# Optimization experiments

Measured on AMD Instinct MI355X. Metric: run time of the kernel, lower is better.

## Reference

```python
import jax, jax.numpy as jnp
import numpy as np

N, E, H, B = 100000, 1600000, 64, 256
EPS = 1e-5


def ln(x, g, b):
    mu = jnp.mean(x, axis=-1, keepdims=True)
    var = jnp.mean((x - mu) ** 2, axis=-1, keepdims=True)
    return (x - mu) * jax.lax.rsqrt(var + EPS) * g + b


def gelu(x):
    # torch nn.GELU default is exact (erf) gelu
    return jax.nn.gelu(x, approximate=False)


def setup_inputs() -> dict:
    key = jax.random.key(0)
    ks = iter(jax.random.split(key, 64))
    nk = lambda: next(ks)
    s = 0.1
    p = {}
    p["x"] = jax.random.normal(nk(), (N, 2), jnp.float32)
    p["edge_attr"] = jax.random.normal(nk(), (E, 2), jnp.float32)
    # node_embed: Linear(2,H) LN GELU Linear(H,H) LN GELU (dropout = eval no-op)
    p["ne_w1"] = jax.random.normal(nk(), (2, H), jnp.float32) * s
    p["ne_b1"] = jnp.zeros((H,), jnp.float32)
    p["ne_g1"] = jnp.ones((H,), jnp.float32)
    p["ne_be1"] = jnp.zeros((H,), jnp.float32)
    p["ne_w2"] = jax.random.normal(nk(), (H, H), jnp.float32) * s
    p["ne_b2"] = jnp.zeros((H,), jnp.float32)
    p["ne_g2"] = jnp.ones((H,), jnp.float32)
    p["ne_be2"] = jnp.zeros((H,), jnp.float32)
    # 3 TrackConv layers: message MLP Linear(H+2,H)+LN, conv output LN, and outer per-layer LN
    p["conv_w"] = jax.random.normal(nk(), (3, H + 2, H), jnp.float32) * s
    p["conv_b"] = jnp.zeros((3, H), jnp.float32)
    p["conv_mg"] = jnp.ones((3, H), jnp.float32)
    p["conv_mb"] = jnp.zeros((3, H), jnp.float32)
    p["conv_ng"] = jnp.ones((3, H), jnp.float32)
    p["conv_nb"] = jnp.zeros((3, H), jnp.float32)
    p["out_ng"] = jnp.ones((3, H), jnp.float32)
    p["out_nb"] = jnp.zeros((3, H), jnp.float32)
    # head MLP: Linear(H,H)+LN+ReLU, Linear(H,H//2)+LN+ReLU, Linear(H//2,1)
    p["m_w1"] = jax.random.normal(nk(), (H, H), jnp.float32) * s
    p["m_b1"] = jnp.zeros((H,), jnp.float32)
    p["m_g1"] = jnp.ones((H,), jnp.float32)
    p["m_be1"] = jnp.zeros((H,), jnp.float32)
    p["m_w2"] = jax.random.normal(nk(), (H, H // 2), jnp.float32) * s
    p["m_b2"] = jnp.zeros((H // 2,), jnp.float32)
    p["m_g2"] = jnp.ones((H // 2,), jnp.float32)
    p["m_be2"] = jnp.zeros((H // 2,), jnp.float32)
    p["m_w3"] = jax.random.normal(nk(), (H // 2, 1), jnp.float32) * s
    p["m_b3"] = jnp.zeros((1,), jnp.float32)
    p["edge_index"] = jax.random.randint(nk(), (2, E), 0, N, dtype=jnp.int32)
    p["batch"] = jnp.sort(jax.random.randint(nk(), (N,), 0, B, dtype=jnp.int32))
    return p


def reference(x, edge_attr,
              ne_w1, ne_b1, ne_g1, ne_be1, ne_w2, ne_b2, ne_g2, ne_be2,
              conv_w, conv_b, conv_mg, conv_mb, conv_ng, conv_nb, out_ng, out_nb,
              m_w1, m_b1, m_g1, m_be1, m_w2, m_b2, m_g2, m_be2, m_w3, m_b3,
              edge_index, batch):
    # node embedding (dropout in eval = identity)
    h = gelu(ln(x @ ne_w1 + ne_b1, ne_g1, ne_be1))
    h = gelu(ln(h @ ne_w2 + ne_b2, ne_g2, ne_be2))
    src, dst = edge_index[0], edge_index[1]  # PyG: message from src (x_j), aggregate at dst
    deg = jax.ops.segment_sum(jnp.ones((E,), h.dtype), dst, num_segments=N)
    deg = jnp.maximum(deg, 1.0)[:, None]
    for l in range(3):
        msg_in = jnp.concatenate([h[src], edge_attr], axis=-1)  # [E, H+2]
        msg = gelu(ln(msg_in @ conv_w[l] + conv_b[l], conv_mg[l], conv_mb[l]))  # [E, H]
        agg = jax.ops.segment_sum(msg, dst, num_segments=N) / deg  # mean aggregate
        conv_out = ln(agg + h, conv_ng[l], conv_nb[l])  # TrackConv: norm(out + residual)
        h = h + ln(conv_out, out_ng[l], out_nb[l])  # outer norm + residual
    # global mean pool over graphs
    cnt = jnp.maximum(jax.ops.segment_sum(jnp.ones((N,), h.dtype), batch, num_segments=B), 1.0)[:, None]
    g = jax.ops.segment_sum(h, batch, num_segments=B) / cnt  # [B, H]
    g = jax.nn.relu(ln(g @ m_w1 + m_b1, m_g1, m_be1))
    g = jax.nn.relu(ln(g @ m_w2 + m_b2, m_g2, m_be2))
    return g @ m_w3 + m_b3  # [B, 1]
```

## Files before the change

### kernel.cpp

```cpp
#include <hip/hip_runtime.h>
#include <math.h>


typedef __attribute__((ext_vector_type(8))) short bfrag;
typedef __attribute__((ext_vector_type(4))) float ffrag;

template <int CTRL>
__device__ __forceinline__ float dpp_mov(float v) {
  return __int_as_float(
      __builtin_amdgcn_update_dpp(0, __float_as_int(v), CTRL, 0xF, 0xF, true));
}

__device__ __forceinline__ float rsum16(float v) {
  v += dpp_mov<0x128>(v);
  v += dpp_mov<0x124>(v);
  v += dpp_mov<0x122>(v);
  v += dpp_mov<0x121>(v);
  return v;
}

__device__ __forceinline__ float wave_sum64(float v) {
  v = rsum16(v);
  v += __shfl_xor(v, 16, 64);
  v += __shfl_xor(v, 32, 64);
  return v;
}

__device__ __forceinline__ float ln_apply(float t, float g, float b) {
  float mu = wave_sum64(t) * 0.015625f;
  float d = t - mu;
  float var = wave_sum64(d * d) * 0.015625f;
  return d * rsqrtf(var + 1e-5f) * g + b;
}

__device__ __forceinline__ float erf_fast(float x) {
  float ax = fabsf(x);
  float p = fmaf(fmaf(fmaf(fmaf(0.078108f, ax, 0.000972f), ax, 0.230389f),
                      ax, 0.278393f), ax, 1.0f);
  p = p * p;
  p = p * p;
  float r = __builtin_amdgcn_rcpf(p);
  return copysignf(1.0f - r, x);
}

__device__ __forceinline__ float gelu_exact(float v) {
  float half = 0.5f * v;
  return fmaf(half, erf_fast(v * 0.70710678118654752440f), half);
}

__device__ __forceinline__ float lane_bcast(float v, int k) {
  return __uint_as_float(__builtin_amdgcn_readlane(__float_as_uint(v), k));
}

__device__ __forceinline__ short f2bf(float f) {
  union { float f; unsigned u; } v; v.f = f;
  unsigned r = v.u + 0x7fffu + ((v.u >> 16) & 1u);
  return (short)(r >> 16);
}

__global__ __launch_bounds__(256) void k_init(
    const float* __restrict__ x,
    const float* __restrict__ w1, const float* __restrict__ b1,
    const float* __restrict__ g1, const float* __restrict__ be1,
    const float* __restrict__ w2, const float* __restrict__ b2,
    const float* __restrict__ g2, const float* __restrict__ be2,
    const float* __restrict__ conv_w, ushort* __restrict__ wt,
    const int* __restrict__ ei, int* __restrict__ csr,
    float* __restrict__ h, ushort* __restrict__ hb,
    int n_nodes, int ne, int oHist, int oEmb, int embWaves) {
  const int bid = blockIdx.x;
  const int tid = threadIdx.x;
  if (bid < oHist) {
    const int i = bid * 256 + tid;
    const int k = i % 96, f = (i / 96) % 64, l = i / (96 * 64);
    const float v = (k < 66) ? conv_w[(size_t)l * 66 * 64 + k * 64 + f] : 0.0f;
    wt[i] = (ushort)f2bf(v);
    return;
  }
  if (bid < oEmb) {
    const int i = (bid - oHist) * 256 + tid;
    if (i < ne) atomicAdd(&csr[ei[ne + i]], 1);
    return;
  }
  const int lane = tid & 63;
  const int wid = ((bid - oEmb) * 256 + tid) >> 6;
  const int nw = embWaves;
  float wc[64];
#pragma unroll
  for (int k = 0; k < 64; k++) wc[k] = w2[k * 64 + lane];
  const float w1a = w1[lane], w1b = w1[64 + lane];
  const float vb1 = b1[lane], vg1 = g1[lane], vbe1 = be1[lane];
  const float vb2 = b2[lane], vg2 = g2[lane], vbe2 = be2[lane];
  for (int n = wid; n < n_nodes; n += nw) {
    const float x0 = x[2 * n], x1 = x[2 * n + 1];
    float t = fmaf(x0, w1a, fmaf(x1, w1b, vb1));
    t = gelu_exact(ln_apply(t, vg1, vbe1));
    float a0 = vb2, a1 = 0.f, a2 = 0.f, a3 = 0.f;
#pragma unroll
    for (int k = 0; k < 64; k += 4) {
      a0 = fmaf(lane_bcast(t, k + 0), wc[k + 0], a0);
      a1 = fmaf(lane_bcast(t, k + 1), wc[k + 1], a1);
      a2 = fmaf(lane_bcast(t, k + 2), wc[k + 2], a2);
      a3 = fmaf(lane_bcast(t, k + 3), wc[k + 3], a3);
    }
    float acc = (a0 + a1) + (a2 + a3);
    acc = gelu_exact(ln_apply(acc, vg2, vbe2));
    h[n * 64 + lane] = acc;
    hb[n * 64 + lane] = (ushort)f2bf(acc);
  }
}

__global__ __launch_bounds__(1024) void k_scan_fast(int* __restrict__ buf, int n) {
  __shared__ int wsum[16];
  const int tid = threadIdx.x, lane = tid & 63, w = tid >> 6;
  const int chunk = (((n + 1023) / 1024) + 3) & ~3;
  const int a = min(tid * chunk, n), b = min(a + chunk, n);
  const bool full = (a + chunk <= n);
  int s = 0;
  if (full) {
    const int4* p4 = (const int4*)(buf + a);
#pragma unroll 4
    for (int i = 0; i < chunk / 4; i++) {
      int4 v = p4[i];
      s += v.x + v.y + v.z + v.w;
    }
  } else {
    for (int i = a; i < b; i++) s += buf[i];
  }
  int inc = s;
#pragma unroll
  for (int sh = 1; sh < 64; sh <<= 1) {
    int t = __shfl_up(inc, sh, 64);
    if (lane >= sh) inc += t;
  }
  if (lane == 63) wsum[w] = inc;
  __syncthreads();
  int wb = 0;
  for (int j = 0; j < w; j++) wb += wsum[j];
  int excl = wb + inc - s;
  if (full) {
    int4* p4 = (int4*)(buf + a);
#pragma unroll 4
    for (int i = 0; i < chunk / 4; i++) {
      int4 v = p4[i];
      int4 o;
      o.x = excl; excl += v.x;
      o.y = excl; excl += v.y;
      o.z = excl; excl += v.z;
      o.w = excl; excl += v.w;
      p4[i] = o;
    }
  } else {
    for (int i = a; i < b; i++) { int v = buf[i]; buf[i] = excl; excl += v; }
  }
}

__global__ void k_scatter(const int* __restrict__ ei, const float* __restrict__ ea,
                          int* __restrict__ cursor, int2* __restrict__ edata, int ne) {
  int i = blockIdx.x * blockDim.x + threadIdx.x;
  if (i < ne) {
    const int d = ei[ne + i];
    const int s = ei[i];
    const float2 eav = *(const float2*)(ea + 2 * (size_t)i);
    const unsigned pk = (unsigned)(ushort)f2bf(eav.x) |
                        ((unsigned)(ushort)f2bf(eav.y) << 16);
    const int pos = atomicAdd(&cursor[d], 1);
    edata[pos] = make_int2(s, (int)pk);
  }
}

__global__ __launch_bounds__(1024) void k_edge_node(
    const float* __restrict__ h_in, const ushort* __restrict__ hb_in,
    float* __restrict__ h_out, ushort* __restrict__ hb_out,
    const int2* __restrict__ edata, const int* __restrict__ ends,
    const ushort* __restrict__ wt,
    const float* __restrict__ bias, const float* __restrict__ mg,
    const float* __restrict__ mb,
    const float* __restrict__ ng, const float* __restrict__ nb,
    const float* __restrict__ og, const float* __restrict__ ob,
    int n_nodes, int writeHb) {
  __shared__ __align__(16) ushort lwt[64 * 96];
  {
    const uint4* s = (const uint4*)wt;
    uint4* d = (uint4*)lwt;
    if (threadIdx.x < 768) d[threadIdx.x] = s[threadIdx.x];
  }
  __syncthreads();

  const int lane = threadIdx.x & 63;
  const int grp = lane >> 4, col = lane & 15;
  const int wid = (blockIdx.x * blockDim.x + threadIdx.x) >> 6;
  const int nw = (gridDim.x * blockDim.x) >> 6;

  float vb[4], vg[4], vbb[4];
#pragma unroll
  for (int t = 0; t < 4; t++) {
    const int f = t * 16 + col;
    vb[t] = bias[f]; vg[t] = mg[f]; vbb[t] = mb[f];
  }

  for (int n = wid; n < n_nodes; n += nw) {
    const int start = (n == 0) ? 0 : ends[n - 1];
    const int end = ends[n];
    float aggf[4] = {0.f, 0.f, 0.f, 0.f};

    int p = start;
    int2 ed = edata[p + min(col, end - p - 1)];
    const ushort* hp0 = hb_in + (size_t)ed.x * 64 + grp * 8;
    bfrag A0 = *(const bfrag*)(hp0);
    bfrag A1 = *(const bfrag*)(hp0 + 32);
    int edy = ed.y;

    for (;;) {
      const int rem = min(16, end - p);
      const int pn = p + 16;
      const bool more = pn < end;
      const int nidx = more ? (pn + min(col, end - pn - 1)) : (p + min(col, rem - 1));
      const int2 edn = edata[nidx];

      bfrag A2 = {0, 0, 0, 0, 0, 0, 0, 0};
      if (grp == 0) {
        A2[0] = (short)(edy & 0xffff);
        A2[1] = (short)((unsigned)edy >> 16);
      }

      ffrag acc[4];
#pragma unroll
      for (int t = 0; t < 4; t++) { ffrag c = {vb[t], vb[t], vb[t], vb[t]}; acc[t] = c; }
#pragma unroll
      for (int t = 0; t < 4; t++) {
        const bfrag B = *(const bfrag*)(lwt + (t * 16 + col) * 96 + grp * 8);
        acc[t] = __builtin_amdgcn_mfma_f32_16x16x32_bf16(A0, B, acc[t], 0, 0, 0);
      }
#pragma unroll
      for (int t = 0; t < 4; t++) {
        const bfrag B = *(const bfrag*)(lwt + (t * 16 + col) * 96 + 32 + grp * 8);
        acc[t] = __builtin_amdgcn_mfma_f32_16x16x32_bf16(A1, B, acc[t], 0, 0, 0);
      }
#pragma unroll
      for (int t = 0; t < 4; t++) {
        const bfrag B = *(const bfrag*)(lwt + (t * 16 + col) * 96 + 64 + grp * 8);
        acc[t] = __builtin_amdgcn_mfma_f32_16x16x32_bf16(A2, B, acc[t], 0, 0, 0);
      }

      const ushort* hq = hb_in + (size_t)edn.x * 64 + grp * 8;
      const bfrag N0 = *(const bfrag*)(hq);
      const bfrag N1 = *(const bfrag*)(hq + 32);

      float sx[4], sq[4];
#pragma unroll
      for (int r = 0; r < 4; r++) {
        float s = (acc[0][r] + acc[1][r]) + (acc[2][r] + acc[3][r]);
        float q = fmaf(acc[0][r], acc[0][r], fmaf(acc[1][r], acc[1][r],
                  fmaf(acc[2][r], acc[2][r], acc[3][r] * acc[3][r])));
        sx[r] = s; sq[r] = q;
      }
#pragma unroll
      for (int r = 0; r < 4; r++) sx[r] = rsum16(sx[r]);
#pragma unroll
      for (int r = 0; r < 4; r++) sq[r] = rsum16(sq[r]);
      float iv[4], mi[4], mk[4];
#pragma unroll
      for (int r = 0; r < 4; r++) {
        const float mu = sx[r] * 0.015625f;
        const float var = fmaf(-mu, mu, sq[r] * 0.015625f);
        iv[r] = rsqrtf(var + 1e-5f);
        mi[r] = -mu * iv[r];
        mk[r] = (grp * 4 + r < rem) ? 1.0f : 0.0f;
      }

#pragma unroll
      for (int t = 0; t < 4; t++) {
        float rs = 0.f;
#pragma unroll
        for (int r = 0; r < 4; r++) {
          const float z = fmaf(acc[t][r], iv[r], mi[r]);
          float v = fmaf(z, vg[t], vbb[t]);
          v = gelu_exact(v);
          rs = fmaf(v, mk[r], rs);
        }
        aggf[t] += rs;
      }

      if (!more) break;
      p = pn; A0 = N0; A1 = N1; edy = edn.y;
    }

#pragma unroll
    for (int t = 0; t < 4; t++) {
      float v = aggf[t];
      v += __shfl_xor(v, 16, 64);
      v += __shfl_xor(v, 32, 64);
      aggf[t] = v;
    }

    const float aggl = (grp == 0) ? aggf[0] : (grp == 1) ? aggf[1]
                     : (grp == 2) ? aggf[2] : aggf[3];

    const float dg = fmaxf((float)(end - start), 1.0f);
    const float hv = h_in[(size_t)n * 64 + lane];
    const float a = aggl / dg + hv;
    const float c = ln_apply(a, ng[lane], nb[lane]);
    const float o = ln_apply(c, og[lane], ob[lane]);
    const float outv = hv + o;
    h_out[(size_t)n * 64 + lane] = outv;
    if (writeHb) hb_out[(size_t)n * 64 + lane] = (ushort)f2bf(outv);
  }
}

__global__ void k_pool_seg(const float* __restrict__ h, const int* __restrict__ batch,
                           float* __restrict__ g, float* __restrict__ cnt,
                           int n_nodes, int chunk) {
  const int lane = threadIdx.x & 63;
  const int wid = (blockIdx.x * blockDim.x + threadIdx.x) >> 6;
  const int n0 = wid * chunk;
  if (n0 >= n_nodes) return;
  const int n1 = min(n0 + chunk, n_nodes);
  int cur = batch[n0], c = 0;
  float acc = 0.f;
  for (int n = n0; n < n1; n++) {
    const int b = batch[n];
    if (b != cur) {
      atomicAdd(&g[(size_t)cur * 64 + lane], acc);
      if (lane == 0) atomicAdd(&cnt[cur], (float)c);
      acc = 0.f; c = 0; cur = b;
    }
    acc += h[(size_t)n * 64 + lane];
    c++;
  }
  atomicAdd(&g[(size_t)cur * 64 + lane], acc);
  if (lane == 0) atomicAdd(&cnt[cur], (float)c);
}

__global__ void k_head(const float* __restrict__ g, const float* __restrict__ cnt,
                       const float* __restrict__ w1, const float* __restrict__ b1,
                       const float* __restrict__ g1, const float* __restrict__ be1,
                       const float* __restrict__ w2, const float* __restrict__ b2,
                       const float* __restrict__ g2, const float* __restrict__ be2,
                       const float* __restrict__ w3, const float* __restrict__ b3,
                       float* __restrict__ out, int nb_) {
  const int lane = threadIdx.x & 63;
  const int row = (blockIdx.x * blockDim.x + threadIdx.x) >> 6;
  if (row >= nb_) return;
  const float c = fmaxf(cnt[row], 1.0f);
  const float gv = g[row * 64 + lane] / c;
  float a0 = b1[lane], a1 = 0.f, a2 = 0.f, a3 = 0.f;
#pragma unroll
  for (int k = 0; k < 64; k += 4) {
    a0 = fmaf(lane_bcast(gv, k + 0), w1[(k + 0) * 64 + lane], a0);
    a1 = fmaf(lane_bcast(gv, k + 1), w1[(k + 1) * 64 + lane], a1);
    a2 = fmaf(lane_bcast(gv, k + 2), w1[(k + 2) * 64 + lane], a2);
    a3 = fmaf(lane_bcast(gv, k + 3), w1[(k + 3) * 64 + lane], a3);
  }
  float t = (a0 + a1) + (a2 + a3);
  t = fmaxf(ln_apply(t, g1[lane], be1[lane]), 0.0f);

  const int j = lane & 31;
  float c0 = b2[j], c1 = 0.f, c2 = 0.f, c3 = 0.f;
#pragma unroll
  for (int k = 0; k < 64; k += 4) {
    c0 = fmaf(lane_bcast(t, k + 0), w2[(k + 0) * 32 + j], c0);
    c1 = fmaf(lane_bcast(t, k + 1), w2[(k + 1) * 32 + j], c1);
    c2 = fmaf(lane_bcast(t, k + 2), w2[(k + 2) * 32 + j], c2);
    c3 = fmaf(lane_bcast(t, k + 3), w2[(k + 3) * 32 + j], c3);
  }
  float t2 = (c0 + c1) + (c2 + c3);
  t2 = fmaxf(ln_apply(t2, g2[j], be2[j]), 0.0f);
  const float p = t2 * w3[j];
  const float s = wave_sum64(p) * 0.5f;
  if (lane == 0) out[row] = s + b3[0];
}

extern "C" void kernel_launch(void* const* d_in, const int* in_sizes, int n_in,
                              void* d_out, int out_size, void* d_ws, size_t ws_size,
                              hipStream_t stream) {
  const float* x      = (const float*)d_in[0];
  const float* ea     = (const float*)d_in[1];
  const float* ne_w1  = (const float*)d_in[2];
  const float* ne_b1  = (const float*)d_in[3];
  const float* ne_g1  = (const float*)d_in[4];
  const float* ne_be1 = (const float*)d_in[5];
  const float* ne_w2  = (const float*)d_in[6];
  const float* ne_b2  = (const float*)d_in[7];
  const float* ne_g2  = (const float*)d_in[8];
  const float* ne_be2 = (const float*)d_in[9];
  const float* conv_w = (const float*)d_in[10];
  const float* conv_b = (const float*)d_in[11];
  const float* conv_mg= (const float*)d_in[12];
  const float* conv_mb= (const float*)d_in[13];
  const float* conv_ng= (const float*)d_in[14];
  const float* conv_nb= (const float*)d_in[15];
  const float* out_ng = (const float*)d_in[16];
  const float* out_nb = (const float*)d_in[17];
  const float* m_w1   = (const float*)d_in[18];
  const float* m_b1   = (const float*)d_in[19];
  const float* m_g1   = (const float*)d_in[20];
  const float* m_be1  = (const float*)d_in[21];
  const float* m_w2   = (const float*)d_in[22];
  const float* m_b2   = (const float*)d_in[23];
  const float* m_g2   = (const float*)d_in[24];
  const float* m_be2  = (const float*)d_in[25];
  const float* m_w3   = (const float*)d_in[26];
  const float* m_b3   = (const float*)d_in[27];
  const int*   eidx   = (const int*)d_in[28];
  const int*   batch  = (const int*)d_in[29];
  float* outp = (float*)d_out;

  const int NN = in_sizes[29];
  const int NE = in_sizes[1] / 2;
  const int NB = out_size;

  float* ws = (float*)d_ws;
  float*  h0   = ws;
  float*  h1   = h0 + (size_t)NN * 64;
  float*  gbuf = h1 + (size_t)NN * 64;
  float*  cnt  = gbuf + (size_t)NB * 64;
  ushort* wt   = (ushort*)(cnt + NB);
  ushort* hb0  = wt + 3 * 64 * 96;
  ushort* hb1  = hb0 + (size_t)NN * 64;
  int*    csr  = (int*)(hb1 + (size_t)NN * 64);
  int2*   edata= (int2*)(csr + NN);

  const dim3 blk(256);

  hipMemsetAsync(csr, 0, sizeof(int) * (size_t)NN, stream);
  hipMemsetAsync(gbuf, 0, sizeof(float) * ((size_t)NB * 64 + NB), stream);

  const int nPrep = (3 * 64 * 96) / 256;
  const int nHist = (NE + 255) / 256;
  const int oHist = nPrep, oEmb = nPrep + nHist;
  const int embBlocks = 2048;
  k_init<<<oEmb + embBlocks, blk, 0, stream>>>(
      x, ne_w1, ne_b1, ne_g1, ne_be1, ne_w2, ne_b2, ne_g2, ne_be2,
      conv_w, wt, eidx, csr, h0, hb0, NN, NE, oHist, oEmb, embBlocks * 4);

  k_scan_fast<<<1, 1024, 0, stream>>>(csr, NN);
  k_scatter<<<(NE + 255) / 256, blk, 0, stream>>>(eidx, ea, csr, edata, NE);

  float* hin = h0;  float* hout = h1;
  ushort* hbin = hb0; ushort* hbout = hb1;
  for (int l = 0; l < 3; l++) {
    k_edge_node<<<1024, dim3(1024), 0, stream>>>(
        hin, hbin, hout, hbout, edata, csr, wt + (size_t)l * 64 * 96,
        conv_b + l * 64, conv_mg + l * 64, conv_mb + l * 64,
        conv_ng + l * 64, conv_nb + l * 64,
        out_ng + l * 64, out_nb + l * 64, NN, (l < 2) ? 1 : 0);
    float* tf = hin; hin = hout; hout = tf;
    ushort* tb = hbin; hbin = hbout; hbout = tb;
  }

  {
    const int chunk = 32;
    const int nwaves = (NN + chunk - 1) / chunk;
    const int nblocks = (nwaves * 64 + 255) / 256;
    k_pool_seg<<<nblocks, blk, 0, stream>>>(hin, batch, gbuf, cnt, NN, chunk);
  }
  k_head<<<(NB + 3) / 4, blk, 0, stream>>>(gbuf, cnt, m_w1, m_b1, m_g1, m_be1,
                                           m_w2, m_b2, m_g2, m_be2, m_w3, m_b3,
                                           outp, NB);
}
```

Measured before the change: 918.8 us.

## Shrink edge-node blocks to 256 threads, one-pass LN stats, merge memsets

The edge/node kernel now launches 4096 blocks of 256 threads with launch bounds (256,3) instead of 1024 blocks of 1024 threads. This changes register allocation and occupancy, and the weight load into LDS becomes a strided loop. LayerNorm computes its sum and sum of squares in one pass, so the two reductions are independent rather than serial, at some risk to numerical accuracy. The CSR range is read as one int2 load, and the CSR buffer is moved next to gbuf so a single memset clears both.

```diff
diff --git a/kernel.cpp b/kernel.cpp
--- a/kernel.cpp
+++ b/kernel.cpp
@@ -27,10 +27,11 @@
 }
 
 __device__ __forceinline__ float ln_apply(float t, float g, float b) {
-  float mu = wave_sum64(t) * 0.015625f;
-  float d = t - mu;
-  float var = wave_sum64(d * d) * 0.015625f;
-  return d * rsqrtf(var + 1e-5f) * g + b;
+  float s1 = wave_sum64(t);
+  float s2 = wave_sum64(t * t);
+  float mu = s1 * 0.015625f;
+  float var = fmaf(-mu, mu, s2 * 0.015625f);
+  return (t - mu) * rsqrtf(var + 1e-5f) * g + b;
 }
 
 __device__ __forceinline__ float erf_fast(float x) {
@@ -169,7 +170,7 @@
   }
 }
 
-__global__ __launch_bounds__(1024) void k_edge_node(
+__global__ __launch_bounds__(256, 3) void k_edge_node(
     const float* __restrict__ h_in, const ushort* __restrict__ hb_in,
     float* __restrict__ h_out, ushort* __restrict__ hb_out,
     const int2* __restrict__ edata, const int* __restrict__ ends,
@@ -183,7 +184,7 @@
   {
     const uint4* s = (const uint4*)wt;
     uint4* d = (uint4*)lwt;
-    if (threadIdx.x < 768) d[threadIdx.x] = s[threadIdx.x];
+    for (int i = threadIdx.x; i < 768; i += 256) d[i] = s[i];
   }
   __syncthreads();
 
@@ -200,8 +201,13 @@
   }
 
   for (int n = wid; n < n_nodes; n += nw) {
-    const int start = (n == 0) ? 0 : ends[n - 1];
-    const int end = ends[n];
+    int start, end;
+    if (n == 0) {
+      start = 0; end = ends[0];
+    } else {
+      const int2 se = *(const int2*)(ends + n - 1);
+      start = se.x; end = se.y;
+    }
     float aggf[4] = {0.f, 0.f, 0.f, 0.f};
 
     int p = start;
@@ -415,16 +421,16 @@
   float*  h1   = h0 + (size_t)NN * 64;
   float*  gbuf = h1 + (size_t)NN * 64;
   float*  cnt  = gbuf + (size_t)NB * 64;
-  ushort* wt   = (ushort*)(cnt + NB);
+  int*    csr  = (int*)(cnt + NB);
+  ushort* wt   = (ushort*)(csr + NN);
   ushort* hb0  = wt + 3 * 64 * 96;
   ushort* hb1  = hb0 + (size_t)NN * 64;
-  int*    csr  = (int*)(hb1 + (size_t)NN * 64);
-  int2*   edata= (int2*)(csr + NN);
+  int2*   edata= (int2*)(hb1 + (size_t)NN * 64);
 
   const dim3 blk(256);
 
-  hipMemsetAsync(csr, 0, sizeof(int) * (size_t)NN, stream);
-  hipMemsetAsync(gbuf, 0, sizeof(float) * ((size_t)NB * 64 + NB), stream);
+  hipMemsetAsync(gbuf, 0, sizeof(float) * ((size_t)NB * 64 + NB) +
+                          sizeof(int) * (size_t)NN, stream);
 
   const int nPrep = (3 * 64 * 96) / 256;
   const int nHist = (NE + 255) / 256;
@@ -440,7 +446,7 @@
   float* hin = h0;  float* hout = h1;
   ushort* hbin = hb0; ushort* hbout = hb1;
   for (int l = 0; l < 3; l++) {
-    k_edge_node<<<1024, dim3(1024), 0, stream>>>(
+    k_edge_node<<<4096, blk, 0, stream>>>(
         hin, hbin, hout, hbout, edata, csr, wt + (size_t)l * 64 * 96,
         conv_b + l * 64, conv_mg + l * 64, conv_mb + l * 64,
         conv_ng + l * 64, conv_nb + l * 64,
```

Result: faster. 817.4 us (-11.0%).
